# Kernel tuning notes

Hardware: AMD Instinct MI355X
Metric: run time of the kernel (lower is better)

Reference implementation:

```python
import jax, jax.numpy as jnp
import numpy as np

VOCAB, EMBED = 50000, 256
MODULES, HEADS, HID = 2, 4, 64
B, S = 8, 2048
LABELS = 16


def setup_inputs() -> dict:
    key = jax.random.key(0)
    ks = jax.random.split(key, 12)
    seqs = jax.random.randint(ks[0], (B, S), 0, VOCAB)
    emb = jax.random.normal(ks[1], (VOCAB, EMBED), jnp.float32) * 0.02
    Wq = jax.random.normal(ks[2], (MODULES, HEADS, HID, EMBED), jnp.float32) * (1.0 / np.sqrt(EMBED))
    bq = jax.random.normal(ks[3], (MODULES, HEADS, HID), jnp.float32) * 0.01
    Wk = jax.random.normal(ks[4], (MODULES, HEADS, HID, EMBED), jnp.float32) * (1.0 / np.sqrt(EMBED))
    bk = jax.random.normal(ks[5], (MODULES, HEADS, HID), jnp.float32) * 0.01
    Wv = jax.random.normal(ks[6], (MODULES, HEADS, HID, EMBED), jnp.float32) * (1.0 / np.sqrt(EMBED))
    bv = jax.random.normal(ks[7], (MODULES, HEADS, HID), jnp.float32) * 0.01
    Wz = jax.random.normal(ks[8], (MODULES, EMBED, HEADS * HID), jnp.float32) * (1.0 / np.sqrt(HEADS * HID))
    bz = jax.random.normal(ks[9], (MODULES, EMBED), jnp.float32) * 0.01
    Wo = jax.random.normal(ks[10], (LABELS, S * EMBED), jnp.float32) * (1.0 / np.sqrt(S * EMBED))
    bo = jax.random.normal(ks[11], (LABELS,), jnp.float32) * 0.01
    return {"seqs": seqs, "emb": emb, "Wq": Wq, "bq": bq, "Wk": Wk, "bk": bk,
            "Wv": Wv, "bv": bv, "Wz": Wz, "bz": bz, "Wo": Wo, "bo": bo}


def _forward(seqs, emb, Wq, bq, Wk, bk, Wv, bv, Wz, bz, Wo, bo):
    x = emb[seqs]  # [B, S, E]
    scale = jnp.float32(EMBED) ** 0.5
    for m in range(MODULES):
        # per-head projections with relu (dropout=0 / eval mode)
        Q = jax.nn.relu(jnp.einsum('bse,hde->bhsd', x, Wq[m]) + bq[m][None, :, None, :])
        K = jax.nn.relu(jnp.einsum('bse,hde->bhsd', x, Wk[m]) + bk[m][None, :, None, :])
        V = jax.nn.relu(jnp.einsum('bse,hde->bhsd', x, Wv[m]) + bv[m][None, :, None, :])
        QK = jnp.einsum('bhsd,bhtd->bhst', Q, K) / scale  # [B,H,S,S]
        # double softmax: first over the query axis (torch dim=1 of [B,S,S]),
        # then over the key axis (torch dim=2)
        A = jax.nn.softmax(QK, axis=2)
        A = jax.nn.softmax(A, axis=3)
        Z = jnp.einsum('bhst,bhtd->bhsd', A, V)  # [B,H,S,HID]
        Zall = jnp.transpose(Z, (0, 2, 1, 3)).reshape(x.shape[0], S, HEADS * HID)
        ZF = jnp.einsum('bsk,ek->bse', Zall, Wz[m]) + bz[m]
        x = ZF + x  # residual (layer_norm=False)
    Xf = x.reshape(x.shape[0], S * EMBED)
    y = jax.nn.sigmoid(Xf @ Wo.T + bo)
    return y


def reference(seqs, emb, Wq, bq, Wk, bk, Wv, bv, Wz, bz, Wo, bo):
    return _forward(seqs, emb, Wq, bq, Wk, bk, Wv, bv, Wz, bz, Wo, bo)
```

## Files before the change

kernel.cpp:

```cpp
#include <hip/hip_runtime.h>
#include <math.h>

#define Bb 8
#define Ss 2048
#define Ee 256
#define Hh 4
#define Dd 64

typedef unsigned short u16;
typedef unsigned int u32;
typedef __attribute__((ext_vector_type(8))) short bf16x8;
typedef __attribute__((ext_vector_type(4))) float f32x4;
typedef __attribute__((ext_vector_type(16))) float f32x16;

__device__ __forceinline__ u16 f2bf(float f) {
  union { float f; u32 u; } c; c.f = f;
  return (u16)((c.u + 0x7FFFu + ((c.u >> 16) & 1u)) >> 16);
}
__device__ __forceinline__ float bf2f(u16 u) {
  union { u32 u; float f; } c; c.u = ((u32)u) << 16;
  return c.f;
}
__device__ __forceinline__ float bf2fs(short s) { return bf2f((u16)s); }
__device__ __forceinline__ float ex2(float x) { return __builtin_amdgcn_exp2f(x); }

__global__ __launch_bounds__(256) void k_w2b(const float* __restrict__ src,
                                             u16* __restrict__ dst) {
  int idx = (blockIdx.x * 256 + threadIdx.x) * 4;
  float4 v = *reinterpret_cast<const float4*>(src + idx);
  ushort4 o;
  o.x = f2bf(v.x); o.y = f2bf(v.y); o.z = f2bf(v.z); o.w = f2bf(v.w);
  *reinterpret_cast<ushort4*>(dst + idx) = o;
}

__global__ __launch_bounds__(256) void k_gather(const int* __restrict__ seqs,
                                                const float* __restrict__ emb,
                                                float* __restrict__ x,
                                                u16* __restrict__ xb) {
  int idx = blockIdx.x * 256 + threadIdx.x;
  int row = idx >> 6, c4 = idx & 63;
  int tok = seqs[row];
  float4 v = reinterpret_cast<const float4*>(emb)[(size_t)tok * 64 + c4];
  reinterpret_cast<float4*>(x)[(size_t)row * 64 + c4] = v;
  ushort4 o;
  o.x = f2bf(v.x); o.y = f2bf(v.y); o.z = f2bf(v.z); o.w = f2bf(v.w);
  reinterpret_cast<ushort4*>(xb)[(size_t)row * 64 + c4] = o;
}

__global__ __launch_bounds__(256) void k_qkvm(const u16* __restrict__ xb,
    const u16* __restrict__ Wqb, const u16* __restrict__ Wkb, const u16* __restrict__ Wvb,
    const float* __restrict__ bq, const float* __restrict__ bk, const float* __restrict__ bv,
    u16* __restrict__ Qf, u16* __restrict__ Kf, u16* __restrict__ Vf, int mod) {
  __shared__ short Xs[128][72];
  __shared__ short Ws[128][72];
  int tid = threadIdx.x;
  int bn = blockIdx.x;
  int arr = bn >> 1, coff = (bn & 1) << 7;
  const u16* W = (arr == 0 ? Wqb : arr == 1 ? Wkb : Wvb) + (size_t)mod * 256 * 256;
  const float* bias = (arr == 0 ? bq : arr == 1 ? bk : bv) + mod * 256;
  u16* Out = (arr == 0 ? Qf : arr == 1 ? Kf : Vf);
  float oscale = (arr == 0) ? 0.0625f * 1.44269504f : 1.0f;
  int s0 = blockIdx.y * 128;
  int lr = tid >> 1, lc = (tid & 1) << 5;
  int w = tid >> 6, lane = tid & 63, ml = lane & 15, q = lane >> 4;
  int sh = (w >> 1) << 6, th = (w & 1) << 6;
  f32x4 acc[4][4] = {};
  for (int k0 = 0; k0 < 256; k0 += 64) {
#pragma unroll
    for (int hh = 0; hh < 4; hh++) {
      *reinterpret_cast<bf16x8*>(&Xs[lr][lc + hh * 8]) =
          *reinterpret_cast<const bf16x8*>(xb + (size_t)(s0 + lr) * Ee + k0 + lc + hh * 8);
      *reinterpret_cast<bf16x8*>(&Ws[lr][lc + hh * 8]) =
          *reinterpret_cast<const bf16x8*>(W + (size_t)(coff + lr) * Ee + k0 + lc + hh * 8);
    }
    __syncthreads();
#pragma unroll
    for (int ks = 0; ks < 2; ks++) {
      bf16x8 af[4], bfr[4];
#pragma unroll
      for (int mt = 0; mt < 4; mt++)
        af[mt] = *reinterpret_cast<const bf16x8*>(&Xs[sh + mt * 16 + ml][ks * 32 + q * 8]);
#pragma unroll
      for (int nt = 0; nt < 4; nt++)
        bfr[nt] = *reinterpret_cast<const bf16x8*>(&Ws[th + nt * 16 + ml][ks * 32 + q * 8]);
#pragma unroll
      for (int mt = 0; mt < 4; mt++)
#pragma unroll
        for (int nt = 0; nt < 4; nt++)
          acc[mt][nt] = __builtin_amdgcn_mfma_f32_16x16x32_bf16(af[mt], bfr[nt], acc[mt][nt], 0, 0, 0);
    }
    __syncthreads();
  }
#pragma unroll
  for (int mt = 0; mt < 4; mt++)
#pragma unroll
    for (int nt = 0; nt < 4; nt++)
#pragma unroll
      for (int r = 0; r < 4; r++) {
        int gm = s0 + sh + mt * 16 + q * 4 + r;
        int cc = coff + th + nt * 16 + ml;
        float v = acc[mt][nt][r] + bias[cc];
        v = (v > 0.f ? v : 0.f) * oscale;
        Out[(size_t)gm * Ee + cc] = f2bf(v);
      }
}

__global__ __launch_bounds__(256) void k_vt(const u16* __restrict__ Vf,
                                            u16* __restrict__ Vt) {
  __shared__ u16 T[64][72];
  int tid = threadIdx.x;
  int t0 = blockIdx.x * 64;
  int z = blockIdx.y;
  int b = z >> 2, h = z & 3;
  int lr = tid >> 2, lc = (tid & 3) << 4;
#pragma unroll
  for (int hh = 0; hh < 2; hh++) {
    bf16x8 v = *reinterpret_cast<const bf16x8*>(
        Vf + (size_t)(b * Ss + t0 + lr) * Ee + h * Dd + lc + hh * 8);
#pragma unroll
    for (int j = 0; j < 8; j++) T[lr][lc + hh * 8 + j] = (u16)v[j];
  }
  __syncthreads();
#pragma unroll
  for (int j = 0; j < 16; j++) {
    Vt[((size_t)z * Dd + lr) * Ss + t0 + lc + j] = T[lc + j][lr];
  }
}

__global__ __launch_bounds__(256) void k_vsum(const u16* __restrict__ Vt,
                                              float* __restrict__ SV,
                                              float* __restrict__ csums) {
  int gi = (blockIdx.y * gridDim.x + blockIdx.x) * 256 + threadIdx.x;
  if (gi < 32 * Ss) csums[gi] = 0.f;
  int z = blockIdx.y;
  int d = blockIdx.x * 4 + (threadIdx.x >> 6);
  int lane = threadIdx.x & 63;
  const u16* row = Vt + ((size_t)z * Dd + d) * Ss;
  float s = 0.f;
#pragma unroll
  for (int it = 0; it < 4; it++) {
    bf16x8 v = *reinterpret_cast<const bf16x8*>(row + it * 512 + lane * 8);
#pragma unroll
    for (int j = 0; j < 8; j++) s += bf2fs(v[j]);
  }
#pragma unroll
  for (int off = 32; off; off >>= 1) s += __shfl_xor(s, off);
  if (lane == 0) SV[(size_t)z * Dd + d] = s;
}

__global__ __launch_bounds__(256, 4) void k_csum(const u16* __restrict__ Qf,
    const u16* __restrict__ Kf, float* __restrict__ csums) {
  __shared__ float csm[2][128];
  int tid = threadIdx.x;
  int lin = (blockIdx.z * 2 + blockIdx.y) * 16 + blockIdx.x;
  int wgid = (lin & 7) * 128 + (lin >> 3);
  int ttile = wgid & 15, shalf = (wgid >> 4) & 1, z = wgid >> 5;
  int b = z >> 2, h = z & 3;
  const u16* Qb = Qf + (size_t)b * Ss * Ee + h * Dd;
  const u16* Kb = Kf + (size_t)b * Ss * Ee + h * Dd;
  int w = tid >> 6, lane = tid & 63, l31 = lane & 31, hi = lane >> 5;
  int sh = (w >> 1) << 6, th = (w & 1) << 6;
  const u16* kr = Kb + (size_t)(ttile * 128 + th + l31) * Ee + hi * 8;
  bf16x8 kb[2][4];
#pragma unroll
  for (int tt = 0; tt < 2; tt++)
#pragma unroll
    for (int kk = 0; kk < 4; kk++)
      kb[tt][kk] = *reinterpret_cast<const bf16x8*>(kr + (size_t)tt * 32 * Ee + kk * 16);
  const u16* Qr0 = Qb + (size_t)(shalf * 1024 + sh + l31) * Ee + hi * 8;
  bf16x8 qc0 = *reinterpret_cast<const bf16x8*>(Qr0);
  bf16x8 qc1 = *reinterpret_cast<const bf16x8*>(Qr0 + 16);
  bf16x8 qc2 = *reinterpret_cast<const bf16x8*>(Qr0 + 32);
  bf16x8 qc3 = *reinterpret_cast<const bf16x8*>(Qr0 + 48);
  float cs0 = 0.f, cs1 = 0.f;
  for (int it = 0; it < 16; it++) {
    int itn = (it + 1) & 15;
    const u16* qnp = Qr0 + (size_t)(((itn >> 1) << 7) + ((itn & 1) << 5)) * Ee;
    bf16x8 qn0 = *reinterpret_cast<const bf16x8*>(qnp);
    bf16x8 qn1 = *reinterpret_cast<const bf16x8*>(qnp + 16);
    bf16x8 qn2 = *reinterpret_cast<const bf16x8*>(qnp + 32);
    bf16x8 qn3 = *reinterpret_cast<const bf16x8*>(qnp + 48);
    f32x16 a0 = {}, a1 = {};
    __builtin_amdgcn_s_setprio(1);
    a0 = __builtin_amdgcn_mfma_f32_32x32x16_bf16(qc0, kb[0][0], a0, 0, 0, 0);
    a1 = __builtin_amdgcn_mfma_f32_32x32x16_bf16(qc0, kb[1][0], a1, 0, 0, 0);
    a0 = __builtin_amdgcn_mfma_f32_32x32x16_bf16(qc1, kb[0][1], a0, 0, 0, 0);
    a1 = __builtin_amdgcn_mfma_f32_32x32x16_bf16(qc1, kb[1][1], a1, 0, 0, 0);
    a0 = __builtin_amdgcn_mfma_f32_32x32x16_bf16(qc2, kb[0][2], a0, 0, 0, 0);
    a1 = __builtin_amdgcn_mfma_f32_32x32x16_bf16(qc2, kb[1][2], a1, 0, 0, 0);
    a0 = __builtin_amdgcn_mfma_f32_32x32x16_bf16(qc3, kb[0][3], a0, 0, 0, 0);
    a1 = __builtin_amdgcn_mfma_f32_32x32x16_bf16(qc3, kb[1][3], a1, 0, 0, 0);
    __builtin_amdgcn_s_setprio(0);
#pragma unroll
    for (int j = 0; j < 16; j++) { cs0 += ex2(a0[j]); cs1 += ex2(a1[j]); }
    qc0 = qn0; qc1 = qn1; qc2 = qn2; qc3 = qn3;
  }
  cs0 += __shfl_xor(cs0, 32);
  cs1 += __shfl_xor(cs1, 32);
  if (lane < 32) {
    csm[w >> 1][th + l31] = cs0;
    csm[w >> 1][th + 32 + l31] = cs1;
  }
  __syncthreads();
  if (tid < 128)
    atomicAdd(&csums[(size_t)z * Ss + ttile * 128 + tid], csm[0][tid] + csm[1][tid]);
}

__global__ void k_llog(float* __restrict__ llic) {
  int i = blockIdx.x * 256 + threadIdx.x;
  llic[i] = -__log2f(llic[i]);
}

__global__ __launch_bounds__(512, 4) void k_att(const u16* __restrict__ Qf,
    const u16* __restrict__ Kf, const u16* __restrict__ Vt,
    const float* __restrict__ llic, const float* __restrict__ SV,
    u16* __restrict__ Zb) {
  __shared__ short Ks[64 * 72];
  __shared__ short Vs[64 * 72];
  __shared__ short A2s[128 * 76];
  __shared__ float rs_s[2][128];
  int tid = threadIdx.x;
  int lin = blockIdx.y * 16 + blockIdx.x;
  int wgid = (lin & 7) * 64 + (lin >> 3);
  int z = wgid >> 4, sblk = wgid & 15;
  int b = z >> 2, h = z & 3;
  const u16* Qb = Qf + (size_t)b * Ss * Ee + h * Dd;
  const u16* Kb = Kf + (size_t)b * Ss * Ee + h * Dd;
  const u16* VtZ = Vt + (size_t)z * Dd * Ss;
  const float* lz = llic + (size_t)z * Ss;
  int s0 = sblk * 128;
  int w = tid >> 6, lane = tid & 63, ml = lane & 15, q = lane >> 4;
  int sq = w >> 1, tq = w & 1;
  int wsd = sq << 5, wt = tq << 5;
  bf16x8 qa[2][2];
#pragma unroll
  for (int ks = 0; ks < 2; ks++)
#pragma unroll
    for (int mt = 0; mt < 2; mt++)
      qa[ks][mt] = *reinterpret_cast<const bf16x8*>(
          Qb + (size_t)(s0 + wsd + mt * 16 + ml) * Ee + ks * 32 + q * 8);
  f32x4 acc2[4] = {};
  f32x4 rsv[2] = {};
  int si = tid & 255, sr = si >> 2, sc = (si & 3) << 4;
  bool isK = tid < 256;
  const u16* kst = Kb + (size_t)sr * Ee + sc;
  const u16* vst = VtZ + (size_t)sr * Ss + sc;
  int sof = sr * 72 + sc;
  for (int t0 = 0; t0 < Ss; t0 += 64) {
    __syncthreads();
    if (isK) {
      *reinterpret_cast<bf16x8*>(&Ks[sof])     = *reinterpret_cast<const bf16x8*>(kst + (size_t)t0 * Ee);
      *reinterpret_cast<bf16x8*>(&Ks[sof + 8]) = *reinterpret_cast<const bf16x8*>(kst + (size_t)t0 * Ee + 8);
    } else {
      *reinterpret_cast<bf16x8*>(&Vs[sof])     = *reinterpret_cast<const bf16x8*>(vst + t0);
      *reinterpret_cast<bf16x8*>(&Vs[sof + 8]) = *reinterpret_cast<const bf16x8*>(vst + t0 + 8);
    }
    __syncthreads();
    f32x4 acc[2][2] = {};
#pragma unroll
    for (int ks = 0; ks < 2; ks++) {
      bf16x8 bf[2];
#pragma unroll
      for (int nt = 0; nt < 2; nt++)
        bf[nt] = *reinterpret_cast<const bf16x8*>(&Ks[(wt + nt * 16 + ml) * 72 + ks * 32 + q * 8]);
#pragma unroll
      for (int mt = 0; mt < 2; mt++)
#pragma unroll
        for (int nt = 0; nt < 2; nt++)
          acc[mt][nt] = __builtin_amdgcn_mfma_f32_16x16x32_bf16(qa[ks][mt], bf[nt], acc[mt][nt], 0, 0, 0);
    }
#pragma unroll
    for (int nt = 0; nt < 2; nt++) {
      float lcv = lz[t0 + wt + nt * 16 + ml];
#pragma unroll
      for (int mt = 0; mt < 2; mt++)
#pragma unroll
        for (int r = 0; r < 4; r++) {
          float e1 = ex2(acc[mt][nt][r] + lcv);
          float p = e1 * (1.f + e1 * (0.5f + e1 * (0.166666667f + e1 * 0.0416666667f)));
          rsv[mt][r] += p;
          union { float f; u32 u; } cv; cv.f = p;
          A2s[(wsd + mt * 16 + q * 4 + r) * 76 + wt + nt * 16 + ml] =
              (short)((cv.u + 0x8000u) >> 16);
        }
    }
    __syncthreads();
#pragma unroll
    for (int ks = 0; ks < 2; ks++) {
      bf16x8 af2 = *reinterpret_cast<const bf16x8*>(&A2s[(w * 16 + ml) * 76 + ks * 32 + q * 8]);
      bf16x8 bv[4];
#pragma unroll
      for (int nt = 0; nt < 4; nt++)
        bv[nt] = *reinterpret_cast<const bf16x8*>(&Vs[(nt * 16 + ml) * 72 + ks * 32 + q * 8]);
#pragma unroll
      for (int nt = 0; nt < 4; nt++)
        acc2[nt] = __builtin_amdgcn_mfma_f32_16x16x32_bf16(af2, bv[nt], acc2[nt], 0, 0, 0);
    }
  }
#pragma unroll
  for (int mt = 0; mt < 2; mt++)
#pragma unroll
    for (int r = 0; r < 4; r++) {
      float v = rsv[mt][r];
      v += __shfl_xor(v, 1); v += __shfl_xor(v, 2);
      v += __shfl_xor(v, 4); v += __shfl_xor(v, 8);
      if (ml == 0) rs_s[tq][wsd + mt * 16 + q * 4 + r] = v;
    }
  __syncthreads();
  const float* SVz = SV + (size_t)z * Dd;
#pragma unroll
  for (int r = 0; r < 4; r++) {
    int row = w * 16 + q * 4 + r;
    float inv = 1.f / (2048.f + rs_s[0][row] + rs_s[1][row]);
#pragma unroll
    for (int nt = 0; nt < 4; nt++) {
      float o = (SVz[nt * 16 + ml] + acc2[nt][r]) * inv;
      Zb[(size_t)(b * Ss + s0 + row) * Ee + h * Dd + nt * 16 + ml] = f2bf(o);
    }
  }
}

__global__ __launch_bounds__(256) void k_zfm(const u16* __restrict__ Zb,
    const u16* __restrict__ Wzb, const float* __restrict__ bzp,
    float* __restrict__ x, u16* __restrict__ xb, int mod) {
  __shared__ short Zs[128][72];
  __shared__ short Ws[128][72];
  int tid = threadIdx.x;
  int coff = blockIdx.x << 7;
  const u16* W = Wzb + (size_t)mod * 256 * 256;
  const float* bias = bzp + mod * Ee;
  int s0 = blockIdx.y * 128;
  int lr = tid >> 1, lc = (tid & 1) << 5;
  int w = tid >> 6, lane = tid & 63, ml = lane & 15, q = lane >> 4;
  int sh = (w >> 1) << 6, th = (w & 1) << 6;
  f32x4 acc[4][4] = {};
  for (int k0 = 0; k0 < 256; k0 += 64) {
#pragma unroll
    for (int hh = 0; hh < 4; hh++) {
      *reinterpret_cast<bf16x8*>(&Zs[lr][lc + hh * 8]) =
          *reinterpret_cast<const bf16x8*>(Zb + (size_t)(s0 + lr) * Ee + k0 + lc + hh * 8);
      *reinterpret_cast<bf16x8*>(&Ws[lr][lc + hh * 8]) =
          *reinterpret_cast<const bf16x8*>(W + (size_t)(coff + lr) * Ee + k0 + lc + hh * 8);
    }
    __syncthreads();
#pragma unroll
    for (int ks = 0; ks < 2; ks++) {
      bf16x8 af[4], bfr[4];
#pragma unroll
      for (int mt = 0; mt < 4; mt++)
        af[mt] = *reinterpret_cast<const bf16x8*>(&Zs[sh + mt * 16 + ml][ks * 32 + q * 8]);
#pragma unroll
      for (int nt = 0; nt < 4; nt++)
        bfr[nt] = *reinterpret_cast<const bf16x8*>(&Ws[th + nt * 16 + ml][ks * 32 + q * 8]);
#pragma unroll
      for (int mt = 0; mt < 4; mt++)
#pragma unroll
        for (int nt = 0; nt < 4; nt++)
          acc[mt][nt] = __builtin_amdgcn_mfma_f32_16x16x32_bf16(af[mt], bfr[nt], acc[mt][nt], 0, 0, 0);
    }
    __syncthreads();
  }
#pragma unroll
  for (int mt = 0; mt < 4; mt++)
#pragma unroll
    for (int nt = 0; nt < 4; nt++)
#pragma unroll
      for (int r = 0; r < 4; r++) {
        int gm = s0 + sh + mt * 16 + q * 4 + r;
        int gn = coff + th + nt * 16 + ml;
        float xv = x[(size_t)gm * Ee + gn] + acc[mt][nt][r] + bias[gn];
        x[(size_t)gm * Ee + gn] = xv;
        xb[(size_t)gm * Ee + gn] = f2bf(xv);
      }
}

__global__ __launch_bounds__(256) void k_final1(const float* __restrict__ x,
    const float* __restrict__ Wo, float* __restrict__ part) {
  int cb = blockIdx.x;
  int b0 = blockIdx.y * 2;
  int tid = threadIdx.x;
  int w = tid >> 6, lane = tid & 63;
  float acc[2][16];
#pragma unroll
  for (int bb = 0; bb < 2; bb++)
#pragma unroll
    for (int l = 0; l < 16; l++) acc[bb][l] = 0.f;
  const float4* x4 = reinterpret_cast<const float4*>(x);
  const float4* w4 = reinterpret_cast<const float4*>(Wo);
#pragma unroll
  for (int it = 0; it < 4; it++) {
    int i = it * 256 + tid;
    float4 xv0 = x4[(size_t)(b0 + 0) * 131072 + cb * 1024 + i];
    float4 xv1 = x4[(size_t)(b0 + 1) * 131072 + cb * 1024 + i];
#pragma unroll
    for (int l = 0; l < 16; l++) {
      float4 wv = w4[(size_t)l * 131072 + cb * 1024 + i];
      acc[0][l] += xv0.x * wv.x + xv0.y * wv.y + xv0.z * wv.z + xv0.w * wv.w;
      acc[1][l] += xv1.x * wv.x + xv1.y * wv.y + xv1.z * wv.z + xv1.w * wv.w;
    }
  }
  __shared__ float red[4][32];
#pragma unroll
  for (int bb = 0; bb < 2; bb++)
#pragma unroll
    for (int l = 0; l < 16; l++) {
      float v = acc[bb][l];
#pragma unroll
      for (int off = 1; off < 64; off <<= 1) v += __shfl_xor(v, off);
      if (lane == 0) red[w][bb * 16 + l] = v;
    }
  __syncthreads();
  if (tid < 32) {
    int lb = tid >> 4, l = tid & 15;
    float s = red[0][tid] + red[1][tid] + red[2][tid] + red[3][tid];
    part[(size_t)((b0 + lb) * 16 + l) * 128 + cb] = s;
  }
}

__global__ void k_final2(const float* __restrict__ part, const float* __restrict__ bo,
                         float* __restrict__ out) {
  int idx = threadIdx.x;
  float s = 0.f;
  for (int c = 0; c < 128; c++) s += part[(size_t)idx * 128 + c];
  s += bo[idx & 15];
  out[idx] = 1.f / (1.f + __expf(-s));
}

extern "C" void kernel_launch(void* const* d_in, const int* in_sizes, int n_in,
                              void* d_out, int out_size, void* d_ws, size_t ws_size,
                              hipStream_t stream) {
  const int*   seqs = (const int*)d_in[0];
  const float* emb  = (const float*)d_in[1];
  const float* Wq   = (const float*)d_in[2];
  const float* bq   = (const float*)d_in[3];
  const float* Wk   = (const float*)d_in[4];
  const float* bk   = (const float*)d_in[5];
  const float* Wv   = (const float*)d_in[6];
  const float* bv   = (const float*)d_in[7];
  const float* Wz   = (const float*)d_in[8];
  const float* bz   = (const float*)d_in[9];
  const float* Wo   = (const float*)d_in[10];
  const float* bo   = (const float*)d_in[11];
  float* out = (float*)d_out;
  float* ws  = (float*)d_ws;

  float* x    = ws;
  u16*   xb   = (u16*)(ws + 4194304);
  u16*   Qf   = (u16*)(ws + 6291456);
  u16*   Kf   = (u16*)(ws + 8388608);
  u16*   Vf   = (u16*)(ws + 10485760);
  u16*   Vt   = (u16*)(ws + 12582912);
  u16*   Zb   = (u16*)(ws + 14680064);
  float* SV   = ws + 16777216;
  u16*   Wqb  = (u16*)(ws + 16787456);
  u16*   Wkb  = (u16*)(ws + 16852992);
  u16*   Wvb  = (u16*)(ws + 16918528);
  u16*   Wzb  = (u16*)(ws + 16984064);
  float* llic = ws + 17049600;
  float* part = ws + 6291456;

  k_gather<<<(Bb * Ss * 64) / 256, 256, 0, stream>>>(seqs, emb, x, xb);
  k_w2b<<<131072 / 1024, 256, 0, stream>>>(Wq, Wqb);
  k_w2b<<<131072 / 1024, 256, 0, stream>>>(Wk, Wkb);
  k_w2b<<<131072 / 1024, 256, 0, stream>>>(Wv, Wvb);
  k_w2b<<<131072 / 1024, 256, 0, stream>>>(Wz, Wzb);

  for (int m = 0; m < 2; m++) {
    k_qkvm<<<dim3(6, 128), 256, 0, stream>>>(xb, Wqb, Wkb, Wvb, bq, bk, bv, Qf, Kf, Vf, m);
    k_vt<<<dim3(32, 32), 256, 0, stream>>>(Vf, Vt);
    k_vsum<<<dim3(16, 32), 256, 0, stream>>>(Vt, SV, llic);
    k_csum<<<dim3(16, 2, 32), 256, 0, stream>>>(Qf, Kf, llic);
    k_llog<<<256, 256, 0, stream>>>(llic);
    k_att<<<dim3(16, 32), 512, 0, stream>>>(Qf, Kf, Vt, llic, SV, Zb);
    k_zfm<<<dim3(2, 128), 256, 0, stream>>>(Zb, Wzb, bz, x, xb, m);
  }

  k_final1<<<dim3(128, 4), 256, 0, stream>>>(x, Wo, part);
  k_final2<<<1, 128, 0, stream>>>(part, bo, out);
}
```

Before: 506.3 us.

## Double-buffer K/V tiles in shared memory with register prefetch in attention kernel

The attention kernel now keeps two shared-memory buffers for the K and V tiles and prefetches the next tile into registers, so global loads overlap the MFMA and exp work of the current chunk. This cuts the per-iteration barriers from three to two. The A2s row stride also changes from 76 to 78 to alter the LDS bank mapping. In exchange, shared-memory use and register pressure go up, which may lower occupancy under the 512x4 launch bounds. The final iteration issues a wrap-around prefetch whose data is never used.

After: 498.1 us. About the same (-1.6%).

```diff
diff --git a/kernel.cpp b/kernel.cpp
--- a/kernel.cpp
+++ b/kernel.cpp
@@ -215,9 +215,9 @@
     const u16* __restrict__ Kf, const u16* __restrict__ Vt,
     const float* __restrict__ llic, const float* __restrict__ SV,
     u16* __restrict__ Zb) {
-  __shared__ short Ks[64 * 72];
-  __shared__ short Vs[64 * 72];
-  __shared__ short A2s[128 * 76];
+  __shared__ short Ks[2][64 * 72];
+  __shared__ short Vs[2][64 * 72];
+  __shared__ short A2s[128 * 78];
   __shared__ float rs_s[2][128];
   int tid = threadIdx.x;
   int lin = blockIdx.y * 16 + blockIdx.x;
@@ -246,57 +246,88 @@
   const u16* kst = Kb + (size_t)sr * Ee + sc;
   const u16* vst = VtZ + (size_t)sr * Ss + sc;
   int sof = sr * 72 + sc;
-  for (int t0 = 0; t0 < Ss; t0 += 64) {
-    __syncthreads();
-    if (isK) {
-      *reinterpret_cast<bf16x8*>(&Ks[sof])     = *reinterpret_cast<const bf16x8*>(kst + (size_t)t0 * Ee);
-      *reinterpret_cast<bf16x8*>(&Ks[sof + 8]) = *reinterpret_cast<const bf16x8*>(kst + (size_t)t0 * Ee + 8);
-    } else {
-      *reinterpret_cast<bf16x8*>(&Vs[sof])     = *reinterpret_cast<const bf16x8*>(vst + t0);
-      *reinterpret_cast<bf16x8*>(&Vs[sof + 8]) = *reinterpret_cast<const bf16x8*>(vst + t0 + 8);
-    }
-    __syncthreads();
-    f32x4 acc[2][2] = {};
-#pragma unroll
-    for (int ks = 0; ks < 2; ks++) {
-      bf16x8 bf[2];
-#pragma unroll
-      for (int nt = 0; nt < 2; nt++)
-        bf[nt] = *reinterpret_cast<const bf16x8*>(&Ks[(wt + nt * 16 + ml) * 72 + ks * 32 + q * 8]);
-#pragma unroll
-      for (int mt = 0; mt < 2; mt++)
-#pragma unroll
-        for (int nt = 0; nt < 2; nt++)
-          acc[mt][nt] = __builtin_amdgcn_mfma_f32_16x16x32_bf16(qa[ks][mt], bf[nt], acc[mt][nt], 0, 0, 0);
-    }
-#pragma unroll
-    for (int nt = 0; nt < 2; nt++) {
-      float lcv = lz[t0 + wt + nt * 16 + ml];
-#pragma unroll
-      for (int mt = 0; mt < 2; mt++)
-#pragma unroll
-        for (int r = 0; r < 4; r++) {
-          float e1 = ex2(acc[mt][nt][r] + lcv);
-          float p = e1 * (1.f + e1 * (0.5f + e1 * (0.166666667f + e1 * 0.0416666667f)));
-          rsv[mt][r] += p;
-          union { float f; u32 u; } cv; cv.f = p;
-          A2s[(wsd + mt * 16 + q * 4 + r) * 76 + wt + nt * 16 + ml] =
-              (short)((cv.u + 0x8000u) >> 16);
-        }
-    }
-    __syncthreads();
-#pragma unroll
-    for (int ks = 0; ks < 2; ks++) {
-      bf16x8 af2 = *reinterpret_cast<const bf16x8*>(&A2s[(w * 16 + ml) * 76 + ks * 32 + q * 8]);
-      bf16x8 bv[4];
-#pragma unroll
-      for (int nt = 0; nt < 4; nt++)
-        bv[nt] = *reinterpret_cast<const bf16x8*>(&Vs[(nt * 16 + ml) * 72 + ks * 32 + q * 8]);
-#pragma unroll
-      for (int nt = 0; nt < 4; nt++)
-        acc2[nt] = __builtin_amdgcn_mfma_f32_16x16x32_bf16(af2, bv[nt], acc2[nt], 0, 0, 0);
-    }
-  }
+  bf16x8 pf0, pf1;
+  if (isK) {
+    *reinterpret_cast<bf16x8*>(&Ks[0][sof])     = *reinterpret_cast<const bf16x8*>(kst);
+    *reinterpret_cast<bf16x8*>(&Ks[0][sof + 8]) = *reinterpret_cast<const bf16x8*>(kst + 8);
+    pf0 = *reinterpret_cast<const bf16x8*>(kst + (size_t)64 * Ee);
+    pf1 = *reinterpret_cast<const bf16x8*>(kst + (size_t)64 * Ee + 8);
+  } else {
+    *reinterpret_cast<bf16x8*>(&Vs[0][sof])     = *reinterpret_cast<const bf16x8*>(vst);
+    *reinterpret_cast<bf16x8*>(&Vs[0][sof + 8]) = *reinterpret_cast<const bf16x8*>(vst + 8);
+    pf0 = *reinterpret_cast<const bf16x8*>(vst + 64);
+    pf1 = *reinterpret_cast<const bf16x8*>(vst + 64 + 8);
+  }
+  __syncthreads();
+
+#define CHUNK(T0, PB) { \
+     \
+    f32x4 acc[2][2] = {}; \
+    _Pragma("unroll") \
+    for (int ks = 0; ks < 2; ks++) { \
+      bf16x8 bfk[2]; \
+      _Pragma("unroll") \
+      for (int nt = 0; nt < 2; nt++) \
+        bfk[nt] = *reinterpret_cast<const bf16x8*>(&Ks[PB][(wt + nt * 16 + ml) * 72 + ks * 32 + q * 8]); \
+      _Pragma("unroll") \
+      for (int mt = 0; mt < 2; mt++) \
+        _Pragma("unroll") \
+        for (int nt = 0; nt < 2; nt++) \
+          acc[mt][nt] = __builtin_amdgcn_mfma_f32_16x16x32_bf16(qa[ks][mt], bfk[nt], acc[mt][nt], 0, 0, 0); \
+    } \
+     \
+    _Pragma("unroll") \
+    for (int nt = 0; nt < 2; nt++) { \
+      float lcv = lz[(T0) + wt + nt * 16 + ml]; \
+      _Pragma("unroll") \
+      for (int mt = 0; mt < 2; mt++) \
+        _Pragma("unroll") \
+        for (int r = 0; r < 4; r++) { \
+          float e1 = ex2(acc[mt][nt][r] + lcv); \
+          float p = e1 * (1.f + e1 * (0.5f + e1 * (0.166666667f + e1 * 0.0416666667f))); \
+          rsv[mt][r] += p; \
+          union { float f; u32 u; } cv; cv.f = p; \
+          A2s[(wsd + mt * 16 + q * 4 + r) * 78 + wt + nt * 16 + ml] = \
+              (short)((cv.u + 0x8000u) >> 16); \
+        } \
+    } \
+    __syncthreads(); \
+     \
+    _Pragma("unroll") \
+    for (int ks = 0; ks < 2; ks++) { \
+      bf16x8 af2 = *reinterpret_cast<const bf16x8*>(&A2s[(w * 16 + ml) * 78 + ks * 32 + q * 8]); \
+      bf16x8 bvv[4]; \
+      _Pragma("unroll") \
+      for (int nt = 0; nt < 4; nt++) \
+        bvv[nt] = *reinterpret_cast<const bf16x8*>(&Vs[PB][(nt * 16 + ml) * 72 + ks * 32 + q * 8]); \
+      _Pragma("unroll") \
+      for (int nt = 0; nt < 4; nt++) \
+        acc2[nt] = __builtin_amdgcn_mfma_f32_16x16x32_bf16(af2, bvv[nt], acc2[nt], 0, 0, 0); \
+    } \
+     \
+    { \
+      int tn = ((T0) + 128) & (Ss - 1); \
+      if (isK) { \
+        *reinterpret_cast<bf16x8*>(&Ks[(PB) ^ 1][sof])     = pf0; \
+        *reinterpret_cast<bf16x8*>(&Ks[(PB) ^ 1][sof + 8]) = pf1; \
+        pf0 = *reinterpret_cast<const bf16x8*>(kst + (size_t)tn * Ee); \
+        pf1 = *reinterpret_cast<const bf16x8*>(kst + (size_t)tn * Ee + 8); \
+      } else { \
+        *reinterpret_cast<bf16x8*>(&Vs[(PB) ^ 1][sof])     = pf0; \
+        *reinterpret_cast<bf16x8*>(&Vs[(PB) ^ 1][sof + 8]) = pf1; \
+        pf0 = *reinterpret_cast<const bf16x8*>(vst + tn); \
+        pf1 = *reinterpret_cast<const bf16x8*>(vst + tn + 8); \
+      } \
+    } \
+    __syncthreads(); \
+  }
+
+  for (int t0 = 0; t0 < Ss; t0 += 128) {
+    CHUNK(t0, 0);
+    CHUNK(t0 + 64, 1);
+  }
+#undef CHUNK
+
 #pragma unroll
   for (int mt = 0; mt < 2; mt++)
 #pragma unroll
```
